# Kernel tuning notes

Measured on AMD Instinct MI355X. Metric: run time of the kernel, lower is better.

Reference implementation:

```python
import jax, jax.numpy as jnp
import numpy as np

B, H, W, C, K, CLASSES = 16, 128, 128, 256, 32, 21
BN_EPS = 1e-3  # keras BatchNormalization default epsilon


def setup_inputs() -> dict:
    key = jax.random.key(0)
    ks = jax.random.split(key, 8)
    sup = 1.0 / np.sqrt(K * C)  # codeword init support from build()
    return {
        "inputs": jax.random.normal(ks[0], (B, H, W, C), jnp.float32),
        "codewords": jax.random.uniform(ks[1], (K, C), jnp.float32, -sup, sup),
        "smoothing": jax.random.uniform(ks[2], (K,), jnp.float32, -1.0, 0.0),
        "bn_gamma": jnp.ones((K,), jnp.float32),
        "bn_beta": jnp.zeros((K,), jnp.float32),
        "bn_mean": 0.1 * jax.random.normal(ks[3], (K,), jnp.float32),
        "bn_var": jax.random.uniform(ks[4], (K,), jnp.float32, 0.5, 1.5),
        "W_enc": jax.random.normal(ks[5], (C, C), jnp.float32) / np.sqrt(C),
        "b_enc": jnp.zeros((C,), jnp.float32),
        "W_se": jax.random.normal(ks[6], (C, CLASSES), jnp.float32) / np.sqrt(C),
        "b_se": jnp.zeros((CLASSES,), jnp.float32),
    }


def reference(inputs, codewords, smoothing, bn_gamma, bn_beta, bn_mean, bn_var,
              W_enc, b_enc, W_se, b_se):
    b, h, w, c = inputs.shape
    x = inputs.reshape(b, h * w, c)  # (B, N, C)
    # scaled-L2 squared distances ||x_n - c_k||^2 without the (B,N,K,C) residual tensor
    x2 = jnp.sum(x * x, axis=-1, keepdims=True)            # (B, N, 1)
    c2 = jnp.sum(codewords * codewords, axis=-1)           # (K,)
    d = x2 - 2.0 * jnp.einsum('bnc,kc->bnk', x, codewords) + c2  # (B, N, K)
    wgt = jax.nn.softmax(d * smoothing, axis=-1)           # (B, N, K)
    # sum_n w_nk (x_n - c_k) = (w^T x) - (sum_n w_nk) c_k
    agg = jnp.einsum('bnk,bnc->bkc', wgt, x) - jnp.sum(wgt, axis=1)[..., None] * codewords  # (B, K, C)
    # BatchNormalization(axis=-2): per-codeword params, inference mode
    bn = (agg - bn_mean[None, :, None]) * jax.lax.rsqrt(bn_var + BN_EPS)[None, :, None]
    bn = bn * bn_gamma[None, :, None] + bn_beta[None, :, None]
    enc = jnp.sum(jax.nn.relu(bn), axis=1)                 # (B, C)
    attn = jax.nn.sigmoid(enc @ W_enc + b_enc)             # (B, C)
    featuremaps_out = attn[:, None, None, :] * inputs       # (B, H, W, C)
    se_out = jax.nn.sigmoid(enc @ W_se + b_se)             # (B, classes)
    return featuremaps_out, se_out
```

## Files before the change

kernel.cpp:

```cpp
#include <hip/hip_runtime.h>
#include <hip/hip_bf16.h>
#include <math.h>

#define Bb 16
#define Hh 128
#define Ww 128
#define Cc 256
#define Kk 32
#define CLASSES 21
#define Nn (Hh*Ww)
#define TILE 256
#define TILES_PER_BATCH (Nn/TILE)
#define BLOCKS_PER_BATCH 32
#define TILES_PER_BLOCK (TILES_PER_BATCH/BLOCKS_PER_BATCH)
#define BN_EPS 1e-3f

#define WS_AGG  0
#define WS_WSUM (Bb*Kk*Cc)
#define WS_ATTN (WS_WSUM + Bb*Kk)
#define WS_TOTAL (WS_ATTN + Bb*Cc)

__global__ __launch_bounds__(256, 2) void k_encode(
    const float* __restrict__ x, const float* __restrict__ cw,
    const float* __restrict__ smo, float* __restrict__ agg,
    float* __restrict__ wsum)
{
    __shared__ float w_lds[Kk][TILE];
    __shared__ float sA[Kk], sB[Kk], sC[Kk];

    const int tid = threadIdx.x;
    const int b   = blockIdx.x / BLOCKS_PER_BATCH;
    const int sub = blockIdx.x % BLOCKS_PER_BATCH;

    if (tid < Kk) {
        float c2 = 0.f;
        const float* row = cw + tid * Cc;
        for (int j = 0; j < Cc; j += 4) {
            float4 v = *(const float4*)(row + j);
            c2 += v.x*v.x + v.y*v.y + v.z*v.z + v.w*v.w;
        }
        float s = smo[tid];
        sA[tid] = s;
        sB[tid] = -2.f * s;
        sC[tid] = c2 * s;
    }

    float acc[Kk];
    float wsacc[Kk];
#pragma unroll
    for (int k = 0; k < Kk; ++k) { acc[k] = 0.f; wsacc[k] = 0.f; }

    __syncthreads();

    const float4* cw4 = (const float4*)cw;

    for (int tt = 0; tt < TILES_PER_BLOCK; ++tt) {
        const int tile = sub + tt * BLOCKS_PER_BATCH;
        const int n0   = tile * TILE;

        const float4* xrow = (const float4*)(x + ((size_t)b * Nn + n0 + tid) * Cc);
        float d[Kk];
#pragma unroll
        for (int k = 0; k < Kk; ++k) d[k] = 0.f;
        float x2 = 0.f;

        for (int j = 0; j < Cc/4; ++j) {
            float4 xv = xrow[j];
            x2 = fmaf(xv.x, xv.x, fmaf(xv.y, xv.y, fmaf(xv.z, xv.z, fmaf(xv.w, xv.w, x2))));
#pragma unroll
            for (int k = 0; k < Kk; ++k) {
                float4 cv = cw4[k * (Cc/4) + j];
                d[k] = fmaf(xv.x, cv.x, fmaf(xv.y, cv.y, fmaf(xv.z, cv.z, fmaf(xv.w, cv.w, d[k]))));
            }
        }

        float m = -1e30f;
#pragma unroll
        for (int k = 0; k < Kk; ++k) {
            d[k] = fmaf(x2, sA[k], fmaf(d[k], sB[k], sC[k]));
            m = fmaxf(m, d[k]);
        }
        float sum = 0.f;
#pragma unroll
        for (int k = 0; k < Kk; ++k) { d[k] = __expf(d[k] - m); sum += d[k]; }
        float inv = 1.f / sum;
#pragma unroll
        for (int k = 0; k < Kk; ++k) w_lds[k][tid] = d[k] * inv;

        __syncthreads();

        const int c = tid;
        const float* xin = x + ((size_t)b * Nn + n0) * Cc + c;
        for (int n4 = 0; n4 < TILE/4; ++n4) {
            float x0 = xin[(n4*4 + 0) * Cc];
            float x1 = xin[(n4*4 + 1) * Cc];
            float x2v = xin[(n4*4 + 2) * Cc];
            float x3 = xin[(n4*4 + 3) * Cc];
#pragma unroll
            for (int k = 0; k < Kk; ++k) {
                float4 wv = *(const float4*)&w_lds[k][n4*4];
                acc[k] = fmaf(wv.x, x0, fmaf(wv.y, x1, fmaf(wv.z, x2v, fmaf(wv.w, x3, acc[k]))));
            }
        }

        if (tid < 64) {
#pragma unroll
            for (int k = 0; k < Kk; ++k) {
                float4 wv = *(const float4*)&w_lds[k][tid*4];
                float s = wv.x + wv.y + wv.z + wv.w;
#pragma unroll
                for (int off = 32; off; off >>= 1) s += __shfl_xor(s, off, 64);
                wsacc[k] += s;
            }
        }
        __syncthreads();
    }

    float* aggb = agg + (size_t)b * Kk * Cc;
#pragma unroll
    for (int k = 0; k < Kk; ++k) atomicAdd(aggb + k * Cc + tid, acc[k]);
    if (tid == 0) {
#pragma unroll
        for (int k = 0; k < Kk; ++k) atomicAdd(wsum + b * Kk + k, wsacc[k]);
    }
}

__global__ __launch_bounds__(256) void k_head(
    const float* __restrict__ agg, const float* __restrict__ wsum,
    const float* __restrict__ cw,
    const float* __restrict__ gamma, const float* __restrict__ beta,
    const float* __restrict__ mean, const float* __restrict__ var,
    const float* __restrict__ W_enc, const float* __restrict__ b_enc,
    const float* __restrict__ W_se, const float* __restrict__ b_se,
    float* __restrict__ attn, float* __restrict__ se_out)
{
    __shared__ float enc[Cc];
    const int b = blockIdx.x, c = threadIdx.x;

    float e = 0.f;
#pragma unroll
    for (int k = 0; k < Kk; ++k) {
        float a = agg[((size_t)b * Kk + k) * Cc + c] - wsum[b * Kk + k] * cw[k * Cc + c];
        float bnv = (a - mean[k]) * (1.0f / sqrtf(var[k] + BN_EPS)) * gamma[k] + beta[k];
        e += fmaxf(bnv, 0.f);
    }
    enc[c] = e;
    __syncthreads();

    float s = b_enc[c];
    for (int j = 0; j < Cc; ++j) s = fmaf(enc[j], W_enc[j * Cc + c], s);
    attn[b * Cc + c] = 1.f / (1.f + __expf(-s));

    if (c < CLASSES) {
        float q = b_se[c];
        for (int j = 0; j < Cc; ++j) q = fmaf(enc[j], W_se[j * CLASSES + c], q);
        se_out[b * CLASSES + c] = 1.f / (1.f + __expf(-q));
    }
}

__global__ __launch_bounds__(256) void k_scale(
    const float4* __restrict__ xin, const float* __restrict__ attn,
    float4* __restrict__ out)
{
    const int total = Bb * Nn * Cc / 4;
    int i = blockIdx.x * 256 + threadIdx.x;
    const int stride = gridDim.x * 256;
    for (; i < total; i += stride) {
        int b  = i >> 20;
        int c4 = i & (Cc/4 - 1);
        float4 a = *(const float4*)(attn + b * Cc + c4 * 4);
        float4 v = xin[i];
        v.x *= a.x; v.y *= a.y; v.z *= a.z; v.w *= a.w;
        out[i] = v;
    }
}

extern "C" void kernel_launch(void* const* d_in, const int* in_sizes, int n_in,
                              void* d_out, int out_size, void* d_ws, size_t ws_size,
                              hipStream_t stream)
{
    const float* x     = (const float*)d_in[0];
    const float* cw    = (const float*)d_in[1];
    const float* smo   = (const float*)d_in[2];
    const float* gamma = (const float*)d_in[3];
    const float* beta  = (const float*)d_in[4];
    const float* mean  = (const float*)d_in[5];
    const float* var   = (const float*)d_in[6];
    const float* W_enc = (const float*)d_in[7];
    const float* b_enc = (const float*)d_in[8];
    const float* W_se  = (const float*)d_in[9];
    const float* b_se  = (const float*)d_in[10];

    float* ws   = (float*)d_ws;
    float* agg  = ws + WS_AGG;
    float* wsum = ws + WS_WSUM;
    float* attn = ws + WS_ATTN;

    float* fm_out = (float*)d_out;
    float* se_out = fm_out + (size_t)Bb * Nn * Cc;

    hipMemsetAsync(d_ws, 0, WS_TOTAL * sizeof(float), stream);

    k_encode<<<Bb * BLOCKS_PER_BATCH, 256, 0, stream>>>(x, cw, smo, agg, wsum);
    k_head<<<Bb, Cc, 0, stream>>>(agg, wsum, cw, gamma, beta, mean, var,
                                  W_enc, b_enc, W_se, b_se, attn, se_out);
    k_scale<<<2048, 256, 0, stream>>>((const float4*)x, attn, (float4*)d_out);
}
```

Baseline: 779.9 us.

## Move encoding GEMMs to split-bf16 MFMA and parallelize head and scale kernels

The scalar-FMA distance and aggregation loops in the encode kernel are replaced with MFMA 16x16x32 bf16 instructions. To keep fp32-like accuracy, each operand is split into high and low bf16 parts and three products are accumulated. x tiles are staged transposed in LDS, and softmax weights are stored in XOR-swizzled LDS. The grid doubles to 64 tiles per batch, the head is split into separate enc/SE and attention kernels, and the scale kernel uses a fixed unrolled chunk per block. The cost is more atomics, more LDS traffic, and a small loss of precision from the bf16x3 emulation.

```diff
diff --git a/kernel.cpp b/kernel.cpp
--- a/kernel.cpp
+++ b/kernel.cpp
@@ -3,158 +3,277 @@
 #include <math.h>
 
 #define Bb 16
-#define Hh 128
-#define Ww 128
 #define Cc 256
 #define Kk 32
 #define CLASSES 21
-#define Nn (Hh*Ww)
-#define TILE 256
-#define TILES_PER_BATCH (Nn/TILE)
-#define BLOCKS_PER_BATCH 32
-#define TILES_PER_BLOCK (TILES_PER_BATCH/BLOCKS_PER_BATCH)
+#define Nn 16384
 #define BN_EPS 1e-3f
 
 #define WS_AGG  0
 #define WS_WSUM (Bb*Kk*Cc)
 #define WS_ATTN (WS_WSUM + Bb*Kk)
-#define WS_TOTAL (WS_ATTN + Bb*Cc)
+#define WS_ENC  (WS_ATTN + Bb*Cc)
+
+typedef float  f32x4  __attribute__((ext_vector_type(4)));
+typedef short  short8 __attribute__((ext_vector_type(8)));
+typedef unsigned int u32;
+
+union Frag { u32 u[4]; short8 s; };
+
+__device__ inline void split2(float a, float b, u32& h, u32& l) {
+    u32 ba = __float_as_uint(a), bb = __float_as_uint(b);
+    float fa = __uint_as_float(ba & 0xFFFF0000u);
+    float fb = __uint_as_float(bb & 0xFFFF0000u);
+    float la = a - fa, lb = b - fb;
+    h = (ba >> 16) | (bb & 0xFFFF0000u);
+    l = (__float_as_uint(la) >> 16) | (__float_as_uint(lb) & 0xFFFF0000u);
+}
+__device__ inline void split8(f32x4 v0, f32x4 v1, Frag& h, Frag& l) {
+    split2(v0[0], v0[1], h.u[0], l.u[0]);
+    split2(v0[2], v0[3], h.u[1], l.u[1]);
+    split2(v1[0], v1[1], h.u[2], l.u[2]);
+    split2(v1[2], v1[3], h.u[3], l.u[3]);
+}
 
 __global__ __launch_bounds__(256, 2) void k_encode(
     const float* __restrict__ x, const float* __restrict__ cw,
     const float* __restrict__ smo, float* __restrict__ agg,
     float* __restrict__ wsum)
 {
-    __shared__ float w_lds[Kk][TILE];
+    __shared__ __align__(16) float xt[Cc][68];
+    __shared__ __align__(16) unsigned short wh[Kk * 64];
+    __shared__ __align__(16) unsigned short wl[Kk * 64];
     __shared__ float sA[Kk], sB[Kk], sC[Kk];
 
-    const int tid = threadIdx.x;
-    const int b   = blockIdx.x / BLOCKS_PER_BATCH;
-    const int sub = blockIdx.x % BLOCKS_PER_BATCH;
+    const int tid  = threadIdx.x;
+    const int lane = tid & 63;
+    const int wv   = tid >> 6;
+    const int b    = blockIdx.x >> 6;
+    const int tile = blockIdx.x & 63;
+    const int l15  = lane & 15;
+    const int lg   = lane >> 4;
 
     if (tid < Kk) {
         float c2 = 0.f;
-        const float* row = cw + tid * Cc;
-        for (int j = 0; j < Cc; j += 4) {
-            float4 v = *(const float4*)(row + j);
-            c2 += v.x*v.x + v.y*v.y + v.z*v.z + v.w*v.w;
+        const f32x4* row = (const f32x4*)(cw + tid * Cc);
+        for (int j = 0; j < Cc/4; ++j) {
+            f32x4 v = row[j];
+            c2 += v[0]*v[0] + v[1]*v[1] + v[2]*v[2] + v[3]*v[3];
         }
         float s = smo[tid];
-        sA[tid] = s;
-        sB[tid] = -2.f * s;
-        sC[tid] = c2 * s;
-    }
-
-    float acc[Kk];
-    float wsacc[Kk];
-#pragma unroll
-    for (int k = 0; k < Kk; ++k) { acc[k] = 0.f; wsacc[k] = 0.f; }
-
-    __syncthreads();
-
-    const float4* cw4 = (const float4*)cw;
-
-    for (int tt = 0; tt < TILES_PER_BLOCK; ++tt) {
-        const int tile = sub + tt * BLOCKS_PER_BATCH;
-        const int n0   = tile * TILE;
-
-        const float4* xrow = (const float4*)(x + ((size_t)b * Nn + n0 + tid) * Cc);
-        float d[Kk];
-#pragma unroll
-        for (int k = 0; k < Kk; ++k) d[k] = 0.f;
-        float x2 = 0.f;
-
-        for (int j = 0; j < Cc/4; ++j) {
-            float4 xv = xrow[j];
-            x2 = fmaf(xv.x, xv.x, fmaf(xv.y, xv.y, fmaf(xv.z, xv.z, fmaf(xv.w, xv.w, x2))));
-#pragma unroll
-            for (int k = 0; k < Kk; ++k) {
-                float4 cv = cw4[k * (Cc/4) + j];
-                d[k] = fmaf(xv.x, cv.x, fmaf(xv.y, cv.y, fmaf(xv.z, cv.z, fmaf(xv.w, cv.w, d[k]))));
-            }
-        }
-
-        float m = -1e30f;
-#pragma unroll
-        for (int k = 0; k < Kk; ++k) {
-            d[k] = fmaf(x2, sA[k], fmaf(d[k], sB[k], sC[k]));
-            m = fmaxf(m, d[k]);
-        }
-        float sum = 0.f;
-#pragma unroll
-        for (int k = 0; k < Kk; ++k) { d[k] = __expf(d[k] - m); sum += d[k]; }
-        float inv = 1.f / sum;
-#pragma unroll
-        for (int k = 0; k < Kk; ++k) w_lds[k][tid] = d[k] * inv;
-
+        sA[tid] = s; sB[tid] = -2.f * s; sC[tid] = c2 * s;
+    }
+
+    f32x4 acc2[4][2];
+#pragma unroll
+    for (int mi = 0; mi < 4; ++mi)
+#pragma unroll
+        for (int nt = 0; nt < 2; ++nt)
+#pragma unroll
+            for (int r = 0; r < 4; ++r) acc2[mi][nt][r] = 0.f;
+
+    for (int sub = 0; sub < 4; ++sub) {
         __syncthreads();
 
-        const int c = tid;
-        const float* xin = x + ((size_t)b * Nn + n0) * Cc + c;
-        for (int n4 = 0; n4 < TILE/4; ++n4) {
-            float x0 = xin[(n4*4 + 0) * Cc];
-            float x1 = xin[(n4*4 + 1) * Cc];
-            float x2v = xin[(n4*4 + 2) * Cc];
-            float x3 = xin[(n4*4 + 3) * Cc];
-#pragma unroll
-            for (int k = 0; k < Kk; ++k) {
-                float4 wv = *(const float4*)&w_lds[k][n4*4];
-                acc[k] = fmaf(wv.x, x0, fmaf(wv.y, x1, fmaf(wv.z, x2v, fmaf(wv.w, x3, acc[k]))));
-            }
-        }
-
-        if (tid < 64) {
-#pragma unroll
-            for (int k = 0; k < Kk; ++k) {
-                float4 wv = *(const float4*)&w_lds[k][tid*4];
-                float s = wv.x + wv.y + wv.z + wv.w;
-#pragma unroll
-                for (int off = 32; off; off >>= 1) s += __shfl_xor(s, off, 64);
-                wsacc[k] += s;
-            }
+        const int pxl = l15 + 16 * wv;
+        const float* xsub = x + ((size_t)b * Nn + tile * 256 + sub * 64 + pxl) * Cc;
+        Frag ah[8], al[8];
+        float x2p = 0.f;
+#pragma unroll
+        for (int kc = 0; kc < 8; ++kc) {
+            const int g = kc * 32 + lg * 8;
+            f32x4 v0 = *(const f32x4*)(xsub + g);
+            f32x4 v1 = *(const f32x4*)(xsub + g + 4);
+            x2p = fmaf(v0[0],v0[0],fmaf(v0[1],v0[1],fmaf(v0[2],v0[2],fmaf(v0[3],v0[3],x2p))));
+            x2p = fmaf(v1[0],v1[0],fmaf(v1[1],v1[1],fmaf(v1[2],v1[2],fmaf(v1[3],v1[3],x2p))));
+            split8(v0, v1, ah[kc], al[kc]);
+#pragma unroll
+            for (int e = 0; e < 4; ++e) {
+                xt[g + e][pxl]     = v0[e];
+                xt[g + 4 + e][pxl] = v1[e];
+            }
+        }
+
+        f32x4 acc1[2];
+#pragma unroll
+        for (int nt = 0; nt < 2; ++nt)
+#pragma unroll
+            for (int r = 0; r < 4; ++r) acc1[nt][r] = 0.f;
+
+#pragma unroll
+        for (int kc = 0; kc < 8; ++kc) {
+#pragma unroll
+            for (int nt = 0; nt < 2; ++nt) {
+                const int k = l15 + 16 * nt;
+                const float* cr = cw + k * Cc + kc * 32 + lg * 8;
+                f32x4 c0 = *(const f32x4*)cr;
+                f32x4 c1 = *(const f32x4*)(cr + 4);
+                Frag bh, bl; split8(c0, c1, bh, bl);
+                acc1[nt] = __builtin_amdgcn_mfma_f32_16x16x32_bf16(ah[kc].s, bh.s, acc1[nt], 0, 0, 0);
+                acc1[nt] = __builtin_amdgcn_mfma_f32_16x16x32_bf16(al[kc].s, bh.s, acc1[nt], 0, 0, 0);
+                acc1[nt] = __builtin_amdgcn_mfma_f32_16x16x32_bf16(ah[kc].s, bl.s, acc1[nt], 0, 0, 0);
+            }
+        }
+
+        x2p += __shfl_xor(x2p, 16, 64);
+        x2p += __shfl_xor(x2p, 32, 64);
+        float x2r[4];
+#pragma unroll
+        for (int r = 0; r < 4; ++r) x2r[r] = __shfl(x2p, lg * 4 + r, 64);
+
+        f32x4 arg[2];
+#pragma unroll
+        for (int nt = 0; nt < 2; ++nt) {
+            const int k = l15 + 16 * nt;
+            const float a_ = sA[k], b_ = sB[k], c_ = sC[k];
+#pragma unroll
+            for (int r = 0; r < 4; ++r)
+                arg[nt][r] = fmaf(x2r[r], a_, fmaf(acc1[nt][r], b_, c_));
+        }
+        f32x4 mx;
+#pragma unroll
+        for (int r = 0; r < 4; ++r) mx[r] = fmaxf(arg[0][r], arg[1][r]);
+#pragma unroll
+        for (int off = 1; off <= 8; off <<= 1)
+#pragma unroll
+            for (int r = 0; r < 4; ++r) mx[r] = fmaxf(mx[r], __shfl_xor(mx[r], off, 64));
+
+        f32x4 e0, e1, es;
+#pragma unroll
+        for (int r = 0; r < 4; ++r) {
+            e0[r] = __expf(arg[0][r] - mx[r]);
+            e1[r] = __expf(arg[1][r] - mx[r]);
+            es[r] = e0[r] + e1[r];
+        }
+#pragma unroll
+        for (int off = 1; off <= 8; off <<= 1)
+#pragma unroll
+            for (int r = 0; r < 4; ++r) es[r] += __shfl_xor(es[r], off, 64);
+
+        float sw[2] = {0.f, 0.f};
+#pragma unroll
+        for (int r = 0; r < 4; ++r) {
+            const float inv = 1.f / es[r];
+            const int px = lg * 4 + r + 16 * wv;
+#pragma unroll
+            for (int nt = 0; nt < 2; ++nt) {
+                const int k = l15 + 16 * nt;
+                const float w = (nt ? e1[r] : e0[r]) * inv;
+                sw[nt] += w;
+                const int pxs = (px & 7) | ((((px >> 3) & 7) ^ (k & 7)) << 3);
+                const u32 wb = __float_as_uint(w);
+                const float whf = __uint_as_float(wb & 0xFFFF0000u);
+                wh[k * 64 + pxs] = (unsigned short)(wb >> 16);
+                wl[k * 64 + pxs] = (unsigned short)(__float_as_uint(w - whf) >> 16);
+            }
+        }
+#pragma unroll
+        for (int nt = 0; nt < 2; ++nt) {
+            sw[nt] += __shfl_xor(sw[nt], 16, 64);
+            sw[nt] += __shfl_xor(sw[nt], 32, 64);
+        }
+        if (lane < 16) {
+            atomicAdd(wsum + b * Kk + lane,      sw[0]);
+            atomicAdd(wsum + b * Kk + lane + 16, sw[1]);
         }
         __syncthreads();
+
+#pragma unroll
+        for (int kc2 = 0; kc2 < 2; ++kc2) {
+            Frag bwh[2], bwl[2];
+#pragma unroll
+            for (int nt = 0; nt < 2; ++nt) {
+                const int k = l15 + 16 * nt;
+                const int u = (kc2 * 4 + lg) ^ (k & 7);
+                bwh[nt] = *(const Frag*)&wh[k * 64 + u * 8];
+                bwl[nt] = *(const Frag*)&wl[k * 64 + u * 8];
+            }
+#pragma unroll
+            for (int mi = 0; mi < 4; ++mi) {
+                const int c = wv * 64 + mi * 16 + l15;
+                const int px0 = kc2 * 32 + lg * 8;
+                f32x4 v0 = *(const f32x4*)&xt[c][px0];
+                f32x4 v1 = *(const f32x4*)&xt[c][px0 + 4];
+                Frag xh, xl; split8(v0, v1, xh, xl);
+#pragma unroll
+                for (int nt = 0; nt < 2; ++nt) {
+                    acc2[mi][nt] = __builtin_amdgcn_mfma_f32_16x16x32_bf16(xh.s, bwh[nt].s, acc2[mi][nt], 0, 0, 0);
+                    acc2[mi][nt] = __builtin_amdgcn_mfma_f32_16x16x32_bf16(xl.s, bwh[nt].s, acc2[mi][nt], 0, 0, 0);
+                    acc2[mi][nt] = __builtin_amdgcn_mfma_f32_16x16x32_bf16(xh.s, bwl[nt].s, acc2[mi][nt], 0, 0, 0);
+                }
+            }
+        }
     }
 
     float* aggb = agg + (size_t)b * Kk * Cc;
 #pragma unroll
-    for (int k = 0; k < Kk; ++k) atomicAdd(aggb + k * Cc + tid, acc[k]);
-    if (tid == 0) {
-#pragma unroll
-        for (int k = 0; k < Kk; ++k) atomicAdd(wsum + b * Kk + k, wsacc[k]);
-    }
-}
-
-__global__ __launch_bounds__(256) void k_head(
+    for (int mi = 0; mi < 4; ++mi)
+#pragma unroll
+        for (int nt = 0; nt < 2; ++nt) {
+            const int k = l15 + 16 * nt;
+            const int cbase = wv * 64 + mi * 16 + lg * 4;
+#pragma unroll
+            for (int r = 0; r < 4; ++r)
+                atomicAdd(aggb + k * Cc + cbase + r, acc2[mi][nt][r]);
+        }
+}
+
+__global__ __launch_bounds__(256) void k_enc(
     const float* __restrict__ agg, const float* __restrict__ wsum,
     const float* __restrict__ cw,
     const float* __restrict__ gamma, const float* __restrict__ beta,
     const float* __restrict__ mean, const float* __restrict__ var,
-    const float* __restrict__ W_enc, const float* __restrict__ b_enc,
     const float* __restrict__ W_se, const float* __restrict__ b_se,
-    float* __restrict__ attn, float* __restrict__ se_out)
+    float* __restrict__ enc_out, float* __restrict__ se_out)
 {
     __shared__ float enc[Cc];
+    __shared__ float red[4 * CLASSES];
     const int b = blockIdx.x, c = threadIdx.x;
 
     float e = 0.f;
 #pragma unroll
     for (int k = 0; k < Kk; ++k) {
         float a = agg[((size_t)b * Kk + k) * Cc + c] - wsum[b * Kk + k] * cw[k * Cc + c];
-        float bnv = (a - mean[k]) * (1.0f / sqrtf(var[k] + BN_EPS)) * gamma[k] + beta[k];
+        float bnv = (a - mean[k]) * rsqrtf(var[k] + BN_EPS) * gamma[k] + beta[k];
         e += fmaxf(bnv, 0.f);
     }
     enc[c] = e;
+    enc_out[b * Cc + c] = e;
     __syncthreads();
 
-    float s = b_enc[c];
-    for (int j = 0; j < Cc; ++j) s = fmaf(enc[j], W_enc[j * Cc + c], s);
-    attn[b * Cc + c] = 1.f / (1.f + __expf(-s));
-
+    if (c < 4 * CLASSES) {
+        const int cls = c % CLASSES, p = c / CLASSES;
+        float q = 0.f;
+        for (int j = p * 64; j < p * 64 + 64; ++j)
+            q = fmaf(enc[j], W_se[j * CLASSES + cls], q);
+        red[c] = q;
+    }
+    __syncthreads();
     if (c < CLASSES) {
-        float q = b_se[c];
-        for (int j = 0; j < Cc; ++j) q = fmaf(enc[j], W_se[j * CLASSES + c], q);
-        se_out[b * CLASSES + c] = 1.f / (1.f + __expf(-q));
+        float s = red[c] + red[c + CLASSES] + red[c + 2*CLASSES] + red[c + 3*CLASSES] + b_se[c];
+        se_out[b * CLASSES + c] = 1.f / (1.f + __expf(-s));
+    }
+}
+
+__global__ __launch_bounds__(256) void k_attn(
+    const float* __restrict__ enc, const float* __restrict__ W_enc,
+    const float* __restrict__ b_enc, float* __restrict__ attn)
+{
+    __shared__ float red[4][64];
+    const int b = blockIdx.x >> 2, cq = blockIdx.x & 3;
+    const int cl = threadIdx.x & 63, jq = threadIdx.x >> 6;
+    const int c = cq * 64 + cl;
+    const float* eb = enc + b * Cc;
+
+    float q = 0.f;
+    for (int j = jq * 64; j < jq * 64 + 64; ++j)
+        q = fmaf(eb[j], W_enc[j * Cc + c], q);
+    red[jq][cl] = q;
+    __syncthreads();
+    if (threadIdx.x < 64) {
+        float s = red[0][threadIdx.x] + red[1][threadIdx.x] + red[2][threadIdx.x]
+                + red[3][threadIdx.x] + b_enc[cq * 64 + threadIdx.x];
+        attn[b * Cc + cq * 64 + threadIdx.x] = 1.f / (1.f + __expf(-s));
     }
 }
 
@@ -162,16 +281,15 @@
     const float4* __restrict__ xin, const float* __restrict__ attn,
     float4* __restrict__ out)
 {
-    const int total = Bb * Nn * Cc / 4;
-    int i = blockIdx.x * 256 + threadIdx.x;
-    const int stride = gridDim.x * 256;
-    for (; i < total; i += stride) {
-        int b  = i >> 20;
-        int c4 = i & (Cc/4 - 1);
-        float4 a = *(const float4*)(attn + b * Cc + c4 * 4);
-        float4 v = xin[i];
+    const int b = blockIdx.x >> 8, chunk = blockIdx.x & 255;
+    const float4 a = *(const float4*)(attn + b * Cc + (threadIdx.x & 63) * 4);
+    size_t base = (size_t)b * (Nn * Cc / 4) + chunk * 4096 + threadIdx.x;
+#pragma unroll
+    for (int it = 0; it < 16; ++it) {
+        size_t idx = base + it * 256;
+        float4 v = xin[idx];
         v.x *= a.x; v.y *= a.y; v.z *= a.z; v.w *= a.w;
-        out[i] = v;
+        out[idx] = v;
     }
 }
 
@@ -195,14 +313,16 @@
     float* agg  = ws + WS_AGG;
     float* wsum = ws + WS_WSUM;
     float* attn = ws + WS_ATTN;
+    float* enc  = ws + WS_ENC;
 
     float* fm_out = (float*)d_out;
     float* se_out = fm_out + (size_t)Bb * Nn * Cc;
 
-    hipMemsetAsync(d_ws, 0, WS_TOTAL * sizeof(float), stream);
-
-    k_encode<<<Bb * BLOCKS_PER_BATCH, 256, 0, stream>>>(x, cw, smo, agg, wsum);
-    k_head<<<Bb, Cc, 0, stream>>>(agg, wsum, cw, gamma, beta, mean, var,
-                                  W_enc, b_enc, W_se, b_se, attn, se_out);
-    k_scale<<<2048, 256, 0, stream>>>((const float4*)x, attn, (float4*)d_out);
-}
+    hipMemsetAsync(d_ws, 0, (size_t)(Bb * Kk * Cc + Bb * Kk) * sizeof(float), stream);
+
+    k_encode<<<Bb * 64, 256, 0, stream>>>(x, cw, smo, agg, wsum);
+    k_enc<<<Bb, 256, 0, stream>>>(agg, wsum, cw, gamma, beta, mean, var,
+                                  W_se, b_se, enc, se_out);
+    k_attn<<<Bb * 4, 256, 0, stream>>>(enc, W_enc, b_enc, attn);
+    k_scale<<<Bb * 256, 256, 0, stream>>>((const float4*)x, attn, (float4*)d_out);
+}
```

Measured after the change: 632.6 us. 18.9% less time.
